# Kernel optimization log

Measured on AMD Instinct MI355X. Metric: run time of the kernel, lower is better.

## Reference

```python
import jax, jax.numpy as jnp
import numpy as np

N = 50000      # users
F_IN = 768     # input features
H = 128        # hidden_dimension == linear_channels
E = 400000     # edges per relation
SQRT_D = float(np.sqrt(H))  # heads=1 -> d = H


def leaky_relu(x):
    return jnp.where(x >= 0, x, 0.01 * x)


def hgt_layer(x, edge_list, Wk, bk, Wq, bq, Wv, bv, rel_params, Wa, ba, skip):
    # x: [N, H]; edge_list: list of [2, E] int arrays (row0=src, row1=dst)
    n = x.shape[0]
    k = x @ Wk + bk
    q = x @ Wq + bq
    v = x @ Wv + bv
    out = jnp.zeros_like(x)
    for ei, (A, M, p) in zip(edge_list, rel_params):
        src, dst = ei[0], ei[1]
        kr = (k @ A)[src]                                  # [E, H] gather
        vr = (v @ M)[src]                                  # [E, H] gather
        alpha = jnp.sum(q[dst] * kr, axis=-1) * p[0] / SQRT_D  # [E]
        amax = jax.ops.segment_max(alpha, dst, num_segments=n)
        ex = jnp.exp(alpha - amax[dst])
        denom = jax.ops.segment_sum(ex, dst, num_segments=n)
        w = ex / denom[dst]                                # segment softmax per dst
        out = out + jax.ops.segment_sum(vr * w[:, None], dst, num_segments=n)
    out = jax.nn.gelu(out, approximate=False) @ Wa + ba
    beta = jax.nn.sigmoid(skip[0])                          # learnable skip gate
    return beta * out + (1.0 - beta) * x


def setup_inputs() -> dict:
    key = jax.random.key(0)
    ks = jax.random.split(key, 16)
    d = {}
    d['features'] = jax.random.normal(ks[0], (N, F_IN), dtype=jnp.float32)
    d['edge_index0'] = jax.random.randint(ks[1], (2, E), 0, N, dtype=jnp.int64)
    d['edge_index1'] = jax.random.randint(ks[2], (2, E), 0, N, dtype=jnp.int64)
    d['W1'] = jax.random.normal(ks[3], (F_IN, H), dtype=jnp.float32) / np.sqrt(F_IN)
    d['b1'] = jnp.zeros((H,), jnp.float32)
    d['Wk'] = jax.random.normal(ks[4], (H, H), dtype=jnp.float32) / np.sqrt(H)
    d['bk'] = jnp.zeros((H,), jnp.float32)
    d['Wq'] = jax.random.normal(ks[5], (H, H), dtype=jnp.float32) / np.sqrt(H)
    d['bq'] = jnp.zeros((H,), jnp.float32)
    d['Wv'] = jax.random.normal(ks[6], (H, H), dtype=jnp.float32) / np.sqrt(H)
    d['bv'] = jnp.zeros((H,), jnp.float32)
    d['A0'] = jax.random.normal(ks[7], (H, H), dtype=jnp.float32) / np.sqrt(H)
    d['M0'] = jax.random.normal(ks[8], (H, H), dtype=jnp.float32) / np.sqrt(H)
    d['p0'] = jnp.ones((1,), jnp.float32)
    d['A1'] = jax.random.normal(ks[9], (H, H), dtype=jnp.float32) / np.sqrt(H)
    d['M1'] = jax.random.normal(ks[10], (H, H), dtype=jnp.float32) / np.sqrt(H)
    d['p1'] = jnp.ones((1,), jnp.float32)
    d['Wa'] = jax.random.normal(ks[11], (H, H), dtype=jnp.float32) / np.sqrt(H)
    d['ba'] = jnp.zeros((H,), jnp.float32)
    d['skip'] = jnp.ones((1,), jnp.float32)
    d['Wo1'] = jax.random.normal(ks[12], (H, 64), dtype=jnp.float32) / np.sqrt(H)
    d['bo1'] = jnp.zeros((64,), jnp.float32)
    d['Wo2'] = jax.random.normal(ks[13], (64, 2), dtype=jnp.float32) / np.sqrt(64)
    d['bo2'] = jnp.zeros((2,), jnp.float32)
    return d


def reference(features, edge_index0, edge_index1, W1, b1, Wk, bk, Wq, bq, Wv, bv,
              A0, M0, p0, A1, M1, p1, Wa, ba, skip, Wo1, bo1, Wo2, bo2):
    edges = [edge_index0, edge_index1]
    rel_params = [(A0, M0, p0), (A1, M1, p1)]
    # linear1 + LeakyReLU (dropout is identity in eval mode)
    x = leaky_relu(features @ W1 + b1)
    # HGT_layer1 applied twice (as in the original forward)
    x = hgt_layer(x, edges, Wk, bk, Wq, bq, Wv, bv, rel_params, Wa, ba, skip)
    x = hgt_layer(x, edges, Wk, bk, Wq, bq, Wv, bv, rel_params, Wa, ba, skip)
    x = leaky_relu(x @ Wo1 + bo1)
    return x @ Wo2 + bo2
```

## Files before the change

kernel.cpp:

```cpp
#include <hip/hip_runtime.h>
#include <math.h>

#define NNODES 50000
#define FIN 768
#define HDIM 128
#define NEDGE 400000
#define NSB 49

typedef _Float16 half8 __attribute__((ext_vector_type(8)));
typedef _Float16 half4 __attribute__((ext_vector_type(4)));
typedef _Float16 half2v __attribute__((ext_vector_type(2)));
typedef float f32x4 __attribute__((ext_vector_type(4)));

__device__ __forceinline__ void gld_lds16(const void* g, void* l) {
    __builtin_amdgcn_global_load_lds((const __attribute__((address_space(1))) unsigned int*)g,
                                     (__attribute__((address_space(3))) unsigned int*)l, 16, 0, 0);
}

__device__ __forceinline__ float gelu1(float x) {
    return 0.5f * x * (1.0f + erff(x * 0.70710678118654752f));
}


__global__ __launch_bounds__(256) void count2_kernel(const int* __restrict__ ei0, const int* __restrict__ ei1,
                                                     int* __restrict__ deg0, int* __restrict__ deg1) {
    int e = blockIdx.x * 256 + threadIdx.x;
    const int* ei = blockIdx.y ? ei1 : ei0;
    int* deg = blockIdx.y ? deg1 : deg0;
    if (e < NEDGE) atomicAdd(&deg[ei[NEDGE + e]], 1);
}

__global__ __launch_bounds__(1024) void scan1_kernel(const int* __restrict__ deg0, const int* __restrict__ deg1,
                                                     int* __restrict__ ptr0, int* __restrict__ ptr1,
                                                     int* __restrict__ sums) {
    const int r = blockIdx.y;
    const int* deg = r ? deg1 : deg0;
    int* ptr = r ? ptr1 : ptr0;
    const int b = blockIdx.x, t = threadIdx.x, i = b * 1024 + t;
    __shared__ int buf[1024];
    int v = (i < NNODES) ? deg[i] : 0;
    buf[t] = v;
    __syncthreads();
    for (int off = 1; off < 1024; off <<= 1) {
        int x = (t >= off) ? buf[t - off] : 0;
        __syncthreads();
        buf[t] += x;
        __syncthreads();
    }
    if (i < NNODES) ptr[i] = buf[t] - v;
    if (t == 1023) sums[r * 64 + b] = buf[1023];
}

__global__ __launch_bounds__(64) void scan2_kernel(int* __restrict__ sums,
                                                   int* __restrict__ ptr0, int* __restrict__ ptr1) {
    const int r = blockIdx.x, t = threadIdx.x;
    int orig = (t < NSB) ? sums[r * 64 + t] : 0;
    int v = orig;
    #pragma unroll
    for (int off = 1; off < 64; off <<= 1) {
        int u = __shfl_up(v, off, 64);
        if (t >= off) v += u;
    }
    if (t < NSB) sums[r * 64 + t] = v - orig;
    if (t == NSB - 1) (r ? ptr1 : ptr0)[NNODES] = v;
}

__global__ __launch_bounds__(1024) void scan3_kernel(const int* __restrict__ sums,
                                                     int* __restrict__ ptr0, int* __restrict__ ptr1) {
    const int r = blockIdx.y;
    int* ptr = r ? ptr1 : ptr0;
    const int i = blockIdx.x * 1024 + threadIdx.x;
    if (i < NNODES) ptr[i] += sums[r * 64 + blockIdx.x];
}

__global__ __launch_bounds__(256) void scatter2_kernel(const int* __restrict__ ei0, const int* __restrict__ ei1,
                                                       const int* __restrict__ ptr0, const int* __restrict__ ptr1,
                                                       int* __restrict__ fill0, int* __restrict__ fill1,
                                                       int* __restrict__ csr0, int* __restrict__ csr1) {
    int e = blockIdx.x * 256 + threadIdx.x;
    const int* ei = blockIdx.y ? ei1 : ei0;
    const int* ptr = blockIdx.y ? ptr1 : ptr0;
    int* fill = blockIdx.y ? fill1 : fill0;
    int* csr = blockIdx.y ? csr1 : csr0;
    if (e < NEDGE) {
        int s = ei[e], d = ei[NEDGE + e];
        int p = atomicAdd(&fill[d], 1);
        csr[ptr[d] + p] = s;
    }
}

__global__ __launch_bounds__(256) void gemm_cmb_kernel(
    const float* __restrict__ Wk, const float* __restrict__ Wv,
    const float* __restrict__ A0v, const float* __restrict__ M0v,
    const float* __restrict__ A1v, const float* __restrict__ M1v,
    float* __restrict__ WkA0, float* __restrict__ WvM0,
    float* __restrict__ WkA1, float* __restrict__ WvM1)
{
    const int z = blockIdx.z;
    const float* A = (z & 1) ? Wv : Wk;
    const float* B = (z == 0) ? A0v : (z == 1) ? M0v : (z == 2) ? A1v : M1v;
    float* C = (z == 0) ? WkA0 : (z == 1) ? WvM0 : (z == 2) ? WkA1 : WvM1;
    const int N = 128, K = 128;
    __shared__ float As[16][64];
    __shared__ float Bs[16][64];
    const int t = threadIdx.x;
    const int tx = t & 15, ty = t >> 4;
    const int bm = blockIdx.x * 64, bn = blockIdx.y * 64;
    const int ar = t >> 2, ac = (t & 3) << 2;
    const int br = t >> 4, bc = (t & 15) << 2;
    float acc[4][4] = {};
    for (int kb = 0; kb < K; kb += 16) {
        float4 av = *reinterpret_cast<const float4*>(A + (size_t)(bm + ar) * K + kb + ac);
        float4 bv = *reinterpret_cast<const float4*>(B + (size_t)(kb + br) * N + bn + bc);
        __syncthreads();
        As[ac + 0][ar] = av.x; As[ac + 1][ar] = av.y; As[ac + 2][ar] = av.z; As[ac + 3][ar] = av.w;
        *reinterpret_cast<float4*>(&Bs[br][bc]) = bv;
        __syncthreads();
        #pragma unroll
        for (int kk = 0; kk < 16; ++kk) {
            float4 a = *reinterpret_cast<const float4*>(&As[kk][ty << 2]);
            float4 b = *reinterpret_cast<const float4*>(&Bs[kk][tx << 2]);
            float am[4] = {a.x, a.y, a.z, a.w};
            float bb[4] = {b.x, b.y, b.z, b.w};
            #pragma unroll
            for (int i = 0; i < 4; ++i)
                #pragma unroll
                for (int j = 0; j < 4; ++j)
                    acc[i][j] = fmaf(am[i], bb[j], acc[i][j]);
        }
    }
    #pragma unroll
    for (int i = 0; i < 4; ++i)
        #pragma unroll
        for (int j = 0; j < 4; ++j)
            C[(size_t)(bm + (ty << 2) + i) * N + bn + (tx << 2) + j] = acc[i][j];
}

__global__ __launch_bounds__(128) void bias_cmb_kernel(
    const float* __restrict__ bk, const float* __restrict__ bv,
    const float* __restrict__ A0v, const float* __restrict__ M0v,
    const float* __restrict__ A1v, const float* __restrict__ M1v,
    float* __restrict__ bqkv)
{
    const int z = blockIdx.x;
    const int j = threadIdx.x;
    const float* b = (z & 1) ? bv : bk;
    const float* Mtx = (z == 0) ? A0v : (z == 1) ? M0v : (z == 2) ? A1v : M1v;
    float s = 0.f;
    for (int i = 0; i < HDIM; ++i) s += b[i] * Mtx[i * HDIM + j];
    const int r = z >> 1, kv = z & 1;
    bqkv[128 + r * 256 + ((j >> 1) << 2) + (kv << 1) + (j & 1)] = s;
}

__global__ __launch_bounds__(128) void pack_qkvT(
    const float* __restrict__ Wq,   const float* __restrict__ WkA0, const float* __restrict__ WvM0,
    const float* __restrict__ WkA1, const float* __restrict__ WvM1,
    const float* __restrict__ bq,
    _Float16* __restrict__ WT, float* __restrict__ bb)
{
    int n = blockIdx.x;
    int k = threadIdx.x;
    int seg = n >> 7, col = n & 127;
    const float* W = (seg == 0) ? Wq : (seg == 1) ? WkA0 : (seg == 2) ? WvM0 : (seg == 3) ? WkA1 : WvM1;
    int np;
    if (seg == 0) np = col;
    else {
        int r = (seg - 1) >> 1, kv = (seg - 1) & 1;
        np = 128 + r * 256 + ((col >> 1) << 2) + (kv << 1) + (col & 1);
    }
    WT[(size_t)np * 128 + k] = (_Float16)W[(size_t)k * 128 + col];
    if (seg == 0 && k == 0) bb[col] = bq[col];
}

__global__ void transpose_h(const float* __restrict__ W, _Float16* __restrict__ WT, int K, int N) {
    int n = blockIdx.x, k = threadIdx.x;
    WT[(size_t)n * K + k] = (_Float16)W[(size_t)k * N + n];
}

template<int MODE, int ATYPE, bool GELU>
__global__ __launch_bounds__(256) void gemm_h(
    const void* __restrict__ Av, const _Float16* __restrict__ Bt,
    const float* __restrict__ bias, const _Float16* __restrict__ Dh,
    const float* __restrict__ gate, _Float16* __restrict__ C,
    int M, int N, int K)
{
    __shared__ _Float16 sA[4096];
    __shared__ _Float16 sB[4096];
    const int t = threadIdx.x;
    const int w = t >> 6, lane = t & 63;
    const int wm = w >> 1, wn = w & 1;
    const int bm = blockIdx.x * 128, bn = blockIdx.y * 128;
    const f32x4 zero = {0.f, 0.f, 0.f, 0.f};
    f32x4 acc[4][4];
    #pragma unroll
    for (int i = 0; i < 4; ++i)
        #pragma unroll
        for (int j = 0; j < 4; ++j) acc[i][j] = zero;

    for (int kb = 0; kb < K; kb += 32) {
        #pragma unroll
        for (int it = 0; it < 2; ++it) {
            const int c = it * 256 + t;
            const int l = c & 63;
            const int row = ((c >> 6) << 4) | (l & 15);
            const int kc = (l >> 4) << 3;
            const int cb = it * 256 + (t & 192);
            int arow = bm + row; if (arow > M - 1) arow = M - 1;
            int brow = bn + row; if (brow > N - 1) brow = N - 1;
            if (ATYPE == 1) {
                const float* ap = (const float*)Av + (size_t)arow * K + kb + kc;
                f32x4 v0 = *(const f32x4*)ap;
                f32x4 v1 = *(const f32x4*)(ap + 4);
                float tmp[8] = {v0[0], v0[1], v0[2], v0[3], v1[0], v1[1], v1[2], v1[3]};
                half8 av;
                #pragma unroll
                for (int j = 0; j < 8; ++j) {
                    float x = tmp[j];
                    if (GELU) x = gelu1(x);
                    av[j] = (_Float16)x;
                }
                *(half8*)(sA + (size_t)c * 8) = av;
            } else if (GELU) {
                half8 hv = *(const half8*)((const _Float16*)Av + (size_t)arow * K + kb + kc);
                half8 av;
                #pragma unroll
                for (int j = 0; j < 8; ++j) av[j] = (_Float16)gelu1((float)hv[j]);
                *(half8*)(sA + (size_t)c * 8) = av;
            } else {
                gld_lds16((const _Float16*)Av + (size_t)arow * K + kb + kc, sA + (size_t)cb * 8);
            }
            gld_lds16(Bt + (size_t)brow * K + kb + kc, sB + (size_t)cb * 8);
        }
        __syncthreads();
        half8 af[4], bf[4];
        #pragma unroll
        for (int i = 0; i < 4; ++i) af[i] = *(const half8*)(sA + ((size_t)((wm * 4 + i) * 64 + lane)) * 8);
        #pragma unroll
        for (int i = 0; i < 4; ++i) bf[i] = *(const half8*)(sB + ((size_t)((wn * 4 + i) * 64 + lane)) * 8);
        #pragma unroll
        for (int i = 0; i < 4; ++i)
            #pragma unroll
            for (int j = 0; j < 4; ++j)
                acc[i][j] = __builtin_amdgcn_mfma_f32_16x16x32_f16(af[i], bf[j], acc[i][j], 0, 0, 0);
        __syncthreads();
    }

    float be = 0.f;
    if (MODE == 2) be = 1.0f / (1.0f + __expf(-gate[0]));
    const int crow0 = bm + wm * 64;
    const int ccol0 = bn + wn * 64;
    #pragma unroll
    for (int i = 0; i < 4; ++i) {
        #pragma unroll
        for (int j = 0; j < 4; ++j) {
            const int col = ccol0 + j * 16 + (lane & 15);
            if (col >= N) continue;
            #pragma unroll
            for (int r = 0; r < 4; ++r) {
                const int row = crow0 + i * 16 + ((lane >> 4) << 2) + r;
                if (row >= M) continue;
                float val = acc[i][j][r] + bias[col];
                if (MODE == 1) val = (val >= 0.f) ? val : 0.01f * val;
                if (MODE == 2) val = be * val + (1.f - be) * (float)Dh[(size_t)row * HDIM + col];
                C[(size_t)row * N + col] = (_Float16)val;
            }
        }
    }
}

template<int MODE, int ATYPE, bool GELU>
__global__ __launch_bounds__(256) void gemm_h32(
    const void* __restrict__ Av, const _Float16* __restrict__ Bt,
    const float* __restrict__ bias, const _Float16* __restrict__ Dh,
    const float* __restrict__ gate, _Float16* __restrict__ C,
    int M, int N, int K)
{
    __shared__ _Float16 sA[4 * 64 * 8];
    __shared__ _Float16 sB[16 * 64 * 8];
    const int t = threadIdx.x;
    const int w = t >> 6, lane = t & 63;
    const int rl = lane & 15, kg = lane >> 4;
    const int bm = blockIdx.x * 32;
    const f32x4 zero = {0.f, 0.f, 0.f, 0.f};
    f32x4 acc[2][2] = {{zero, zero}, {zero, zero}};

    for (int kb = 0; kb < K; kb += 64) {
        {
            const int mi = w >> 1, kk = w & 1;
            int arow = bm + mi * 16 + rl; if (arow > M - 1) arow = M - 1;
            const int ko = kb + kk * 32 + kg * 8;
            if (ATYPE == 1) {
                const float* ap = (const float*)Av + (size_t)arow * K + ko;
                f32x4 v0 = *(const f32x4*)ap;
                f32x4 v1 = *(const f32x4*)(ap + 4);
                float tmp[8] = {v0[0], v0[1], v0[2], v0[3], v1[0], v1[1], v1[2], v1[3]};
                half8 av;
                #pragma unroll
                for (int j = 0; j < 8; ++j) {
                    float x = tmp[j];
                    if (GELU) x = gelu1(x);
                    av[j] = (_Float16)x;
                }
                *(half8*)(sA + (size_t)(w * 64 + lane) * 8) = av;
            } else if (GELU) {
                half8 hv = *(const half8*)((const _Float16*)Av + (size_t)arow * K + ko);
                half8 av;
                #pragma unroll
                for (int j = 0; j < 8; ++j) av[j] = (_Float16)gelu1((float)hv[j]);
                *(half8*)(sA + (size_t)(w * 64 + lane) * 8) = av;
            } else {
                gld_lds16((const _Float16*)Av + (size_t)arow * K + ko, sA + (size_t)(w * 64) * 8);
            }
        }
        #pragma unroll
        for (int j = 0; j < 4; ++j) {
            const int fb = w * 4 + j;
            const int ni = (j >> 1) & 1, kk = j & 1;
            int nrow = w * 32 + ni * 16 + rl; if (nrow > N - 1) nrow = N - 1;
            gld_lds16(Bt + (size_t)nrow * K + kb + kk * 32 + kg * 8, sB + (size_t)(fb * 64) * 8);
        }
        __syncthreads();
        half8 af[2][2], bf[2][2];
        #pragma unroll
        for (int mi = 0; mi < 2; ++mi)
            #pragma unroll
            for (int kk = 0; kk < 2; ++kk)
                af[mi][kk] = *(const half8*)(sA + (size_t)((mi * 2 + kk) * 64 + lane) * 8);
        #pragma unroll
        for (int ni = 0; ni < 2; ++ni)
            #pragma unroll
            for (int kk = 0; kk < 2; ++kk)
                bf[ni][kk] = *(const half8*)(sB + (size_t)((w * 4 + ni * 2 + kk) * 64 + lane) * 8);
        #pragma unroll
        for (int mi = 0; mi < 2; ++mi)
            #pragma unroll
            for (int ni = 0; ni < 2; ++ni)
                #pragma unroll
                for (int kk = 0; kk < 2; ++kk)
                    acc[mi][ni] = __builtin_amdgcn_mfma_f32_16x16x32_f16(af[mi][kk], bf[ni][kk], acc[mi][ni], 0, 0, 0);
        __syncthreads();
    }

    float be = 0.f;
    if (MODE == 2) be = 1.0f / (1.0f + __expf(-gate[0]));
    #pragma unroll
    for (int mi = 0; mi < 2; ++mi) {
        #pragma unroll
        for (int ni = 0; ni < 2; ++ni) {
            const int col = w * 32 + ni * 16 + rl;
            if (col >= N) continue;
            #pragma unroll
            for (int r = 0; r < 4; ++r) {
                const int row = bm + mi * 16 + kg * 4 + r;
                if (row >= M) continue;
                float val = acc[mi][ni][r] + bias[col];
                if (MODE == 1) val = (val >= 0.f) ? val : 0.01f * val;
                if (MODE == 2) val = be * val + (1.f - be) * (float)Dh[(size_t)row * HDIM + col];
                C[(size_t)row * N + col] = (_Float16)val;
            }
        }
    }
}

__global__ __launch_bounds__(256) void attn2_kernel(
    const _Float16* __restrict__ qkv,
    const int* __restrict__ ptr0, const int* __restrict__ csr0,
    const int* __restrict__ ptr1, const int* __restrict__ csr1,
    const float* __restrict__ p0, const float* __restrict__ p1,
    _Float16* __restrict__ att)
{
    const int w = (blockIdx.x * 256 + threadIdx.x) >> 6;
    if (w >= NNODES) return;
    const int lane = threadIdx.x & 63;
    half2v qh = *(const half2v*)(qkv + (size_t)w * 640 + (lane << 1));
    const float qx = (float)qh[0], qy = (float)qh[1];
    float ox = 0.f, oy = 0.f;
    #pragma unroll
    for (int r = 0; r < 2; ++r) {
        const int* ptrv = r ? ptr1 : ptr0;
        const int* csr  = r ? csr1 : csr0;
        const float scale = (r ? p1[0] : p0[0]) * 0.08838834764831845f;
        const int start = ptrv[w], end = ptrv[w + 1];
        if (start == end) continue;
        const _Float16* tbl = qkv + 128 + 256 * r + (lane << 2);
        float denom = 0.f, ax = 0.f, ay = 0.f;
        int i = start;
        for (; i + 8 <= end; i += 8) {
            int s[8];
            #pragma unroll
            for (int j = 0; j < 8; ++j) s[j] = csr[i + j];
            half4 kv[8];
            #pragma unroll
            for (int j = 0; j < 8; ++j) kv[j] = *(const half4*)(tbl + (size_t)s[j] * 640);
            float d[8];
            #pragma unroll
            for (int j = 0; j < 8; ++j) d[j] = qx * (float)kv[j][0] + qy * (float)kv[j][1];
            #pragma unroll
            for (int o2 = 32; o2; o2 >>= 1) {
                #pragma unroll
                for (int j = 0; j < 8; ++j) d[j] += __shfl_xor(d[j], o2, 64);
            }
            #pragma unroll
            for (int j = 0; j < 8; ++j) {
                const float e = __expf(d[j] * scale);
                denom += e;
                ax += e * (float)kv[j][2];
                ay += e * (float)kv[j][3];
            }
        }
        for (; i + 4 <= end; i += 4) {
            const int s0 = csr[i], s1 = csr[i + 1], s2 = csr[i + 2], s3 = csr[i + 3];
            half4 kv0 = *(const half4*)(tbl + (size_t)s0 * 640);
            half4 kv1 = *(const half4*)(tbl + (size_t)s1 * 640);
            half4 kv2 = *(const half4*)(tbl + (size_t)s2 * 640);
            half4 kv3 = *(const half4*)(tbl + (size_t)s3 * 640);
            float d0 = qx * (float)kv0[0] + qy * (float)kv0[1];
            float d1 = qx * (float)kv1[0] + qy * (float)kv1[1];
            float d2 = qx * (float)kv2[0] + qy * (float)kv2[1];
            float d3 = qx * (float)kv3[0] + qy * (float)kv3[1];
            #pragma unroll
            for (int o2 = 32; o2; o2 >>= 1) {
                d0 += __shfl_xor(d0, o2, 64);
                d1 += __shfl_xor(d1, o2, 64);
                d2 += __shfl_xor(d2, o2, 64);
                d3 += __shfl_xor(d3, o2, 64);
            }
            const float e0 = __expf(d0 * scale), e1 = __expf(d1 * scale);
            const float e2 = __expf(d2 * scale), e3 = __expf(d3 * scale);
            denom += (e0 + e1) + (e2 + e3);
            ax += e0 * (float)kv0[2] + e1 * (float)kv1[2] + e2 * (float)kv2[2] + e3 * (float)kv3[2];
            ay += e0 * (float)kv0[3] + e1 * (float)kv1[3] + e2 * (float)kv2[3] + e3 * (float)kv3[3];
        }
        for (; i < end; ++i) {
            const int s = csr[i];
            half4 kv = *(const half4*)(tbl + (size_t)s * 640);
            float d = qx * (float)kv[0] + qy * (float)kv[1];
            #pragma unroll
            for (int o2 = 32; o2; o2 >>= 1) d += __shfl_xor(d, o2, 64);
            const float e = __expf(d * scale);
            denom += e;
            ax += e * (float)kv[2];
            ay += e * (float)kv[3];
        }
        const float inv = 1.0f / denom;
        ox += ax * inv; oy += ay * inv;
    }
    half2v o;
    o[0] = (_Float16)ox;
    o[1] = (_Float16)oy;
    *(half2v*)(att + (size_t)w * HDIM + (lane << 1)) = o;
}

__global__ __launch_bounds__(256) void head2_kernel(const _Float16* __restrict__ h,
                                                    const float* __restrict__ Wo2,
                                                    const float* __restrict__ bo2,
                                                    float* __restrict__ out)
{
    int i = blockIdx.x * 256 + threadIdx.x;
    if (i >= NNODES) return;
    const _Float16* hp = h + (size_t)i * 64;
    float s0 = bo2[0], s1 = bo2[1];
    #pragma unroll
    for (int j0 = 0; j0 < 64; j0 += 8) {
        half8 hv = *(const half8*)(hp + j0);
        #pragma unroll
        for (int j = 0; j < 8; ++j) {
            float v = (float)hv[j];
            s0 += v * Wo2[2 * (j0 + j)];
            s1 += v * Wo2[2 * (j0 + j) + 1];
        }
    }
    out[2 * i] = s0;
    out[2 * i + 1] = s1;
}


extern "C" void kernel_launch(void* const* d_in, const int* in_sizes, int n_in,
                              void* d_out, int out_size, void* d_ws, size_t ws_size,
                              hipStream_t stream)
{
    const float* features = (const float*)d_in[0];
    const int* ei0 = (const int*)d_in[1];
    const int* ei1 = (const int*)d_in[2];
    const float* W1 = (const float*)d_in[3];
    const float* b1 = (const float*)d_in[4];
    const float* Wk = (const float*)d_in[5];
    const float* bk = (const float*)d_in[6];
    const float* Wq = (const float*)d_in[7];
    const float* bq = (const float*)d_in[8];
    const float* Wv = (const float*)d_in[9];
    const float* bv = (const float*)d_in[10];
    const float* A0 = (const float*)d_in[11];
    const float* M0 = (const float*)d_in[12];
    const float* p0 = (const float*)d_in[13];
    const float* A1 = (const float*)d_in[14];
    const float* M1 = (const float*)d_in[15];
    const float* p1 = (const float*)d_in[16];
    const float* Wa = (const float*)d_in[17];
    const float* ba = (const float*)d_in[18];
    const float* skip = (const float*)d_in[19];
    const float* Wo1 = (const float*)d_in[20];
    const float* bo1 = (const float*)d_in[21];
    const float* Wo2 = (const float*)d_in[22];
    const float* bo2 = (const float*)d_in[23];
    (void)in_sizes; (void)n_in; (void)out_size; (void)ws_size;

    char* base = (char*)d_ws;
    size_t off = 0;
    auto alloc = [&](size_t bytes) { size_t r = off; off = (off + bytes + 255) & ~(size_t)255; return base + r; };

    _Float16* x0h  = (_Float16*)alloc((size_t)NNODES * HDIM * 2);
    _Float16* x1h  = (_Float16*)alloc((size_t)NNODES * HDIM * 2);
    _Float16* qkv  = (_Float16*)alloc((size_t)NNODES * 640 * 2);
    _Float16* att  = (_Float16*)alloc((size_t)NNODES * HDIM * 2);
    _Float16* hh   = (_Float16*)alloc((size_t)NNODES * 64 * 2);
    float* WkA[2]  = { (float*)alloc(65536), (float*)alloc(65536) };
    float* WvM[2]  = { (float*)alloc(65536), (float*)alloc(65536) };
    _Float16* WqkvT = (_Float16*)alloc(640 * 128 * 2);
    float*    bqkv  = (float*)   alloc(640 * 4);
    _Float16* W1T   = (_Float16*)alloc(128 * 768 * 2);
    _Float16* WaT   = (_Float16*)alloc(128 * 128 * 2);
    _Float16* Wo1T  = (_Float16*)alloc(64 * 128 * 2);
    int* deg[2]  = { (int*)alloc(NNODES * 4), (int*)alloc(NNODES * 4) };
    int* ptrv[2] = { (int*)alloc((NNODES + 1) * 4), (int*)alloc((NNODES + 1) * 4) };
    int* fill[2] = { (int*)alloc(NNODES * 4), (int*)alloc(NNODES * 4) };
    int* csr[2]  = { (int*)alloc(NEDGE * 4),  (int*)alloc(NEDGE * 4) };
    int* sums    = (int*)alloc(2 * 64 * 4);

    hipMemsetAsync(deg[0], 0, NNODES * 4, stream);
    hipMemsetAsync(deg[1], 0, NNODES * 4, stream);
    hipMemsetAsync(fill[0], 0, NNODES * 4, stream);
    hipMemsetAsync(fill[1], 0, NNODES * 4, stream);
    const int egrid = (NEDGE + 255) / 256;
    count2_kernel<<<dim3(egrid, 2), 256, 0, stream>>>(ei0, ei1, deg[0], deg[1]);
    scan1_kernel<<<dim3(NSB, 2), 1024, 0, stream>>>(deg[0], deg[1], ptrv[0], ptrv[1], sums);
    scan2_kernel<<<2, 64, 0, stream>>>(sums, ptrv[0], ptrv[1]);
    scan3_kernel<<<dim3(NSB, 2), 1024, 0, stream>>>(sums, ptrv[0], ptrv[1]);
    scatter2_kernel<<<dim3(egrid, 2), 256, 0, stream>>>(ei0, ei1, ptrv[0], ptrv[1],
                                                        fill[0], fill[1], csr[0], csr[1]);

    gemm_cmb_kernel<<<dim3(2, 2, 4), 256, 0, stream>>>(Wk, Wv, A0, M0, A1, M1,
                                                       WkA[0], WvM[0], WkA[1], WvM[1]);
    bias_cmb_kernel<<<4, 128, 0, stream>>>(bk, bv, A0, M0, A1, M1, bqkv);

    pack_qkvT<<<640, 128, 0, stream>>>(Wq, WkA[0], WvM[0], WkA[1], WvM[1], bq, WqkvT, bqkv);
    transpose_h<<<128, 768, 0, stream>>>(W1, W1T, 768, 128);
    transpose_h<<<128, 128, 0, stream>>>(Wa, WaT, 128, 128);
    transpose_h<<<64, 128, 0, stream>>>(Wo1, Wo1T, 128, 64);

    const int MBLK = (NNODES + 127) / 128;
    const int MBLK32 = (NNODES + 31) / 32;

    gemm_h32<1, 1, false><<<MBLK32, 256, 0, stream>>>(
        features, W1T, b1, nullptr, nullptr, x0h, NNODES, HDIM, FIN);

    _Float16* xin = x0h;
    _Float16* xout = x1h;
    for (int layer = 0; layer < 2; ++layer) {
        gemm_h<0, 0, false><<<dim3(MBLK, 5), 256, 0, stream>>>(
            xin, WqkvT, bqkv, nullptr, nullptr, qkv, NNODES, 640, HDIM);
        attn2_kernel<<<(NNODES * 64 + 255) / 256, 256, 0, stream>>>(
            qkv, ptrv[0], csr[0], ptrv[1], csr[1], p0, p1, att);
        gemm_h32<2, 0, true><<<MBLK32, 256, 0, stream>>>(
            att, WaT, ba, xin, skip, xout, NNODES, HDIM, HDIM);
        _Float16* tmp = xin; xin = xout; xout = tmp;
    }

    gemm_h32<1, 0, false><<<MBLK32, 256, 0, stream>>>(
        xin, Wo1T, bo1, nullptr, nullptr, hh, NNODES, 64, HDIM);
    head2_kernel<<<(NNODES + 255) / 256, 256, 0, stream>>>(hh, Wo2, bo2, (float*)d_out);
}
```

Baseline: 469.3 us.

## Merge setup kernels and memsets, use 128-row GEMM for first linear

Folds the bias-combination kernel into the weight-combination kernel as an extra z-slice. The three transposes and the QKV pack become one kernel, and the four memsets become one, which cuts launch count and the per-launch gaps between them. It also switches the 768-wide input projection from the 32-row gemm_h32 tile to the 128-row gemm_h tile. That trades more reuse per block for fewer blocks (391 vs 1563) on the largest GEMM.

```diff
diff --git a/kernel.cpp b/kernel.cpp
--- a/kernel.cpp
+++ b/kernel.cpp
@@ -89,14 +89,30 @@
     }
 }
 
-__global__ __launch_bounds__(256) void gemm_cmb_kernel(
+__global__ __launch_bounds__(256) void cmb_all_kernel(
     const float* __restrict__ Wk, const float* __restrict__ Wv,
+    const float* __restrict__ bk, const float* __restrict__ bv,
     const float* __restrict__ A0v, const float* __restrict__ M0v,
     const float* __restrict__ A1v, const float* __restrict__ M1v,
     float* __restrict__ WkA0, float* __restrict__ WvM0,
-    float* __restrict__ WkA1, float* __restrict__ WvM1)
+    float* __restrict__ WkA1, float* __restrict__ WvM1,
+    float* __restrict__ bqkv)
 {
     const int z = blockIdx.z;
+    if (z == 4) {
+        if (blockIdx.x || blockIdx.y) return;
+        const int j = threadIdx.x;
+        if (j >= 128) return;
+        #pragma unroll
+        for (int zz = 0; zz < 4; ++zz) {
+            const float* b = (zz & 1) ? bv : bk;
+            const float* Mtx = (zz == 0) ? A0v : (zz == 1) ? M0v : (zz == 2) ? A1v : M1v;
+            float s = 0.f;
+            for (int i = 0; i < HDIM; ++i) s += b[i] * Mtx[i * HDIM + j];
+            bqkv[128 + (zz >> 1) * 256 + ((j >> 1) << 2) + ((zz & 1) << 1) + (j & 1)] = s;
+        }
+        return;
+    }
     const float* A = (z & 1) ? Wv : Wk;
     const float* B = (z == 0) ? A0v : (z == 1) ? M0v : (z == 2) ? A1v : M1v;
     float* C = (z == 0) ? WkA0 : (z == 1) ? WvM0 : (z == 2) ? WkA1 : WvM1;
@@ -111,17 +127,17 @@
     float acc[4][4] = {};
     for (int kb = 0; kb < K; kb += 16) {
         float4 av = *reinterpret_cast<const float4*>(A + (size_t)(bm + ar) * K + kb + ac);
-        float4 bv = *reinterpret_cast<const float4*>(B + (size_t)(kb + br) * N + bn + bc);
+        float4 bv2 = *reinterpret_cast<const float4*>(B + (size_t)(kb + br) * N + bn + bc);
         __syncthreads();
         As[ac + 0][ar] = av.x; As[ac + 1][ar] = av.y; As[ac + 2][ar] = av.z; As[ac + 3][ar] = av.w;
-        *reinterpret_cast<float4*>(&Bs[br][bc]) = bv;
+        *reinterpret_cast<float4*>(&Bs[br][bc]) = bv2;
         __syncthreads();
         #pragma unroll
         for (int kk = 0; kk < 16; ++kk) {
             float4 a = *reinterpret_cast<const float4*>(&As[kk][ty << 2]);
-            float4 b = *reinterpret_cast<const float4*>(&Bs[kk][tx << 2]);
+            float4 b2 = *reinterpret_cast<const float4*>(&Bs[kk][tx << 2]);
             float am[4] = {a.x, a.y, a.z, a.w};
-            float bb[4] = {b.x, b.y, b.z, b.w};
+            float bb[4] = {b2.x, b2.y, b2.z, b2.w};
             #pragma unroll
             for (int i = 0; i < 4; ++i)
                 #pragma unroll
@@ -136,45 +152,37 @@
             C[(size_t)(bm + (ty << 2) + i) * N + bn + (tx << 2) + j] = acc[i][j];
 }
 
-__global__ __launch_bounds__(128) void bias_cmb_kernel(
-    const float* __restrict__ bk, const float* __restrict__ bv,
-    const float* __restrict__ A0v, const float* __restrict__ M0v,
-    const float* __restrict__ A1v, const float* __restrict__ M1v,
-    float* __restrict__ bqkv)
-{
-    const int z = blockIdx.x;
-    const int j = threadIdx.x;
-    const float* b = (z & 1) ? bv : bk;
-    const float* Mtx = (z == 0) ? A0v : (z == 1) ? M0v : (z == 2) ? A1v : M1v;
-    float s = 0.f;
-    for (int i = 0; i < HDIM; ++i) s += b[i] * Mtx[i * HDIM + j];
-    const int r = z >> 1, kv = z & 1;
-    bqkv[128 + r * 256 + ((j >> 1) << 2) + (kv << 1) + (j & 1)] = s;
-}
-
-__global__ __launch_bounds__(128) void pack_qkvT(
+__global__ __launch_bounds__(128) void pack_all_kernel(
     const float* __restrict__ Wq,   const float* __restrict__ WkA0, const float* __restrict__ WvM0,
     const float* __restrict__ WkA1, const float* __restrict__ WvM1,
-    const float* __restrict__ bq,
-    _Float16* __restrict__ WT, float* __restrict__ bb)
-{
-    int n = blockIdx.x;
-    int k = threadIdx.x;
-    int seg = n >> 7, col = n & 127;
-    const float* W = (seg == 0) ? Wq : (seg == 1) ? WkA0 : (seg == 2) ? WvM0 : (seg == 3) ? WkA1 : WvM1;
-    int np;
-    if (seg == 0) np = col;
-    else {
-        int r = (seg - 1) >> 1, kv = (seg - 1) & 1;
-        np = 128 + r * 256 + ((col >> 1) << 2) + (kv << 1) + (col & 1);
-    }
-    WT[(size_t)np * 128 + k] = (_Float16)W[(size_t)k * 128 + col];
-    if (seg == 0 && k == 0) bb[col] = bq[col];
-}
-
-__global__ void transpose_h(const float* __restrict__ W, _Float16* __restrict__ WT, int K, int N) {
-    int n = blockIdx.x, k = threadIdx.x;
-    WT[(size_t)n * K + k] = (_Float16)W[(size_t)k * N + n];
+    const float* __restrict__ bq,   const float* __restrict__ W1,
+    const float* __restrict__ Wa,   const float* __restrict__ Wo1,
+    _Float16* __restrict__ WqkvT, float* __restrict__ bqkv,
+    _Float16* __restrict__ W1T, _Float16* __restrict__ WaT, _Float16* __restrict__ Wo1T)
+{
+    const int b = blockIdx.x, k = threadIdx.x;
+    if (b < 640) {
+        int seg = b >> 7, col = b & 127;
+        const float* W = (seg == 0) ? Wq : (seg == 1) ? WkA0 : (seg == 2) ? WvM0 : (seg == 3) ? WkA1 : WvM1;
+        int np;
+        if (seg == 0) np = col;
+        else {
+            int r = (seg - 1) >> 1, kv = (seg - 1) & 1;
+            np = 128 + r * 256 + ((col >> 1) << 2) + (kv << 1) + (col & 1);
+        }
+        WqkvT[(size_t)np * 128 + k] = (_Float16)W[(size_t)k * 128 + col];
+        if (seg == 0 && k == 0) bqkv[col] = bq[col];
+    } else if (b < 768) {
+        const int n = b - 640;
+        for (int kk = k; kk < 768; kk += 128)
+            W1T[(size_t)n * 768 + kk] = (_Float16)W1[(size_t)kk * 128 + n];
+    } else if (b < 896) {
+        const int n = b - 768;
+        WaT[(size_t)n * 128 + k] = (_Float16)Wa[(size_t)k * 128 + n];
+    } else {
+        const int n = b - 896;
+        Wo1T[(size_t)n * 128 + k] = (_Float16)Wo1[(size_t)k * 64 + n];
+    }
 }
 
 template<int MODE, int ATYPE, bool GELU>
@@ -521,16 +529,14 @@
     _Float16* W1T   = (_Float16*)alloc(128 * 768 * 2);
     _Float16* WaT   = (_Float16*)alloc(128 * 128 * 2);
     _Float16* Wo1T  = (_Float16*)alloc(64 * 128 * 2);
-    int* deg[2]  = { (int*)alloc(NNODES * 4), (int*)alloc(NNODES * 4) };
+    int* zb = (int*)alloc((size_t)4 * NNODES * 4);
+    int* deg[2]  = { zb,               zb + NNODES };
+    int* fill[2] = { zb + 2 * NNODES,  zb + 3 * NNODES };
     int* ptrv[2] = { (int*)alloc((NNODES + 1) * 4), (int*)alloc((NNODES + 1) * 4) };
-    int* fill[2] = { (int*)alloc(NNODES * 4), (int*)alloc(NNODES * 4) };
     int* csr[2]  = { (int*)alloc(NEDGE * 4),  (int*)alloc(NEDGE * 4) };
     int* sums    = (int*)alloc(2 * 64 * 4);
 
-    hipMemsetAsync(deg[0], 0, NNODES * 4, stream);
-    hipMemsetAsync(deg[1], 0, NNODES * 4, stream);
-    hipMemsetAsync(fill[0], 0, NNODES * 4, stream);
-    hipMemsetAsync(fill[1], 0, NNODES * 4, stream);
+    hipMemsetAsync(zb, 0, (size_t)4 * NNODES * 4, stream);
     const int egrid = (NEDGE + 255) / 256;
     count2_kernel<<<dim3(egrid, 2), 256, 0, stream>>>(ei0, ei1, deg[0], deg[1]);
     scan1_kernel<<<dim3(NSB, 2), 1024, 0, stream>>>(deg[0], deg[1], ptrv[0], ptrv[1], sums);
@@ -539,19 +545,17 @@
     scatter2_kernel<<<dim3(egrid, 2), 256, 0, stream>>>(ei0, ei1, ptrv[0], ptrv[1],
                                                         fill[0], fill[1], csr[0], csr[1]);
 
-    gemm_cmb_kernel<<<dim3(2, 2, 4), 256, 0, stream>>>(Wk, Wv, A0, M0, A1, M1,
-                                                       WkA[0], WvM[0], WkA[1], WvM[1]);
-    bias_cmb_kernel<<<4, 128, 0, stream>>>(bk, bv, A0, M0, A1, M1, bqkv);
-
-    pack_qkvT<<<640, 128, 0, stream>>>(Wq, WkA[0], WvM[0], WkA[1], WvM[1], bq, WqkvT, bqkv);
-    transpose_h<<<128, 768, 0, stream>>>(W1, W1T, 768, 128);
-    transpose_h<<<128, 128, 0, stream>>>(Wa, WaT, 128, 128);
-    transpose_h<<<64, 128, 0, stream>>>(Wo1, Wo1T, 128, 64);
+    cmb_all_kernel<<<dim3(2, 2, 5), 256, 0, stream>>>(Wk, Wv, bk, bv, A0, M0, A1, M1,
+                                                      WkA[0], WvM[0], WkA[1], WvM[1], bqkv);
+
+    pack_all_kernel<<<960, 128, 0, stream>>>(Wq, WkA[0], WvM[0], WkA[1], WvM[1],
+                                             bq, W1, Wa, Wo1,
+                                             WqkvT, bqkv, W1T, WaT, Wo1T);
 
     const int MBLK = (NNODES + 127) / 128;
     const int MBLK32 = (NNODES + 31) / 32;
 
-    gemm_h32<1, 1, false><<<MBLK32, 256, 0, stream>>>(
+    gemm_h<1, 1, false><<<dim3(MBLK, 1), 256, 0, stream>>>(
         features, W1T, b1, nullptr, nullptr, x0h, NNODES, HDIM, FIN);
 
     _Float16* xin = x0h;
```

Result: faster. 448.4 us (-4.4%).
